# Performance work log

Measured on AMD Instinct MI355X. Metric: run time of the kernel, lower is better.

## Reference

```python
import jax, jax.numpy as jnp
import numpy as np

HID, HEADS, DH, L, OUT = 128, 8, 16, 2, 64
NQ, NA, E, IN = 50000, 50000, 400000, 128
SCALE = float(1.0 / np.sqrt(DH))


def _seg_softmax(alpha, dst, n):
    # softmax over incoming edges of each destination node
    amax = jax.ops.segment_max(alpha, dst, num_segments=n)
    ex = jnp.exp(alpha - amax[dst])
    den = jax.ops.segment_sum(ex, dst, num_segments=n)
    return ex / den[dst]


def _msg(k_src, v_src, q_dst, ei, ar, mr, pr, n_dst):
    # HGTConv message passing for one edge type.
    src, dst = ei[0], ei[1]
    ke = jnp.einsum('ehd,hdf->ehf', k_src[src], ar)  # relation-specific key transform [E,H,DH]
    ve = jnp.einsum('ehd,hdf->ehf', v_src[src], mr)  # relation-specific value transform [E,H,DH]
    alpha = (q_dst[dst] * ke).sum(-1) * pr * SCALE   # [E,H]
    attn = _seg_softmax(alpha, dst, n_dst)
    return jax.ops.segment_sum(attn[..., None] * ve, dst, num_segments=n_dst)  # [n_dst,H,DH]


def setup_inputs():
    key = jax.random.key(0)
    ks = jax.random.split(key, 24)
    f = lambda k, shp: jax.random.normal(k, shp, jnp.float32) * 0.05
    zb = lambda shp: jnp.zeros(shp, jnp.float32)
    return dict(
        x_q=jax.random.normal(ks[0], (NQ, IN), jnp.float32),
        x_a=jax.random.normal(ks[1], (NA, IN), jnp.float32),
        lin0_wq=f(ks[2], (IN, HID)), lin0_bq=zb((HID,)),
        lin0_wa=f(ks[3], (IN, HID)), lin0_ba=zb((HID,)),
        kw_q=f(ks[4], (L, HID, HID)), kb_q=zb((L, HID)),
        qw_q=f(ks[5], (L, HID, HID)), qb_q=zb((L, HID)),
        vw_q=f(ks[6], (L, HID, HID)), vb_q=zb((L, HID)),
        aw_q=f(ks[7], (L, HID, HID)), ab_q=zb((L, HID)),
        kw_a=f(ks[8], (L, HID, HID)), kb_a=zb((L, HID)),
        qw_a=f(ks[9], (L, HID, HID)), qb_a=zb((L, HID)),
        vw_a=f(ks[10], (L, HID, HID)), vb_a=zb((L, HID)),
        aw_a=f(ks[11], (L, HID, HID)), ab_a=zb((L, HID)),
        skip_q=jnp.ones((L,), jnp.float32),
        skip_a=jnp.ones((L,), jnp.float32),
        a_rel=f(ks[12], (L, 2, HEADS, DH, DH)) + jnp.eye(DH, dtype=jnp.float32),
        m_rel=f(ks[13], (L, 2, HEADS, DH, DH)) + jnp.eye(DH, dtype=jnp.float32),
        p_rel=jnp.ones((L, 2, HEADS), jnp.float32),
        lin_w=f(ks[14], (HID, OUT)), lin_b=zb((OUT,)),
        ei_qa=jax.random.randint(ks[15], (2, E), 0, NQ),
        ei_aq=jax.random.randint(ks[16], (2, E), 0, NA),
    )


def reference(x_q, x_a, lin0_wq, lin0_bq, lin0_wa, lin0_ba,
              kw_q, kb_q, qw_q, qb_q, vw_q, vb_q, aw_q, ab_q,
              kw_a, kb_a, qw_a, qb_a, vw_a, vb_a, aw_a, ab_a,
              skip_q, skip_a, a_rel, m_rel, p_rel, lin_w, lin_b,
              ei_qa, ei_aq):
    # per-type input projection + relu
    xq = jax.nn.relu(x_q @ lin0_wq + lin0_bq)
    xa = jax.nn.relu(x_a @ lin0_wa + lin0_ba)
    for l in range(L):
        kq = (xq @ kw_q[l] + kb_q[l]).reshape(NQ, HEADS, DH)
        qq = (xq @ qw_q[l] + qb_q[l]).reshape(NQ, HEADS, DH)
        vq = (xq @ vw_q[l] + vb_q[l]).reshape(NQ, HEADS, DH)
        ka = (xa @ kw_a[l] + kb_a[l]).reshape(NA, HEADS, DH)
        qa = (xa @ qw_a[l] + qb_a[l]).reshape(NA, HEADS, DH)
        va = (xa @ vw_a[l] + vb_a[l]).reshape(NA, HEADS, DH)
        # edge type 0: question -> answer ; edge type 1: answer -> question; group='sum'
        out_a = _msg(kq, vq, qa, ei_qa, a_rel[l, 0], m_rel[l, 0], p_rel[l, 0], NA).reshape(NA, HID)
        out_q = _msg(ka, va, qq, ei_aq, a_rel[l, 1], m_rel[l, 1], p_rel[l, 1], NQ).reshape(NQ, HID)
        oq = jax.nn.gelu(out_q, approximate=False) @ aw_q[l] + ab_q[l]
        oa = jax.nn.gelu(out_a, approximate=False) @ aw_a[l] + ab_a[l]
        gq = jax.nn.sigmoid(skip_q[l])
        ga = jax.nn.sigmoid(skip_a[l])
        xq = gq * oq + (1.0 - gq) * xq
        xa = ga * oa + (1.0 - ga) * xa
    zq = xq @ lin_w + lin_b
    za = xa @ lin_w + lin_b
    # z_dict concatenated: rows [0,NQ) = question, [NQ,NQ+NA) = answer
    return jnp.concatenate([zq, za], axis=0)
```

## Files before the change

### kernel.cpp

```cpp
#include <hip/hip_runtime.h>
#include <hip/hip_bf16.h>
#include <math.h>

typedef __attribute__((ext_vector_type(8))) _Float16 half8;
typedef __attribute__((ext_vector_type(4))) float f32x4;
typedef unsigned short u16;
typedef unsigned int u32;

__device__ __forceinline__ u16 f2h(float f) {
    union { _Float16 h; u16 u; } c; c.h = (_Float16)f; return c.u;
}
__device__ __forceinline__ float h2f(u16 u) {
    union { u16 u; _Float16 h; } c; c.u = u; return (float)c.h;
}
__device__ __forceinline__ float bf2f(u16 u) {
    union { u32 i; float f; } x; x.i = ((u32)u) << 16; return x.f;
}
__device__ __forceinline__ u16 f2bf(float f) {
    union { float f; u32 i; } u; u.f = f;
    u32 r = u.i + 0x7fffu + ((u.i >> 16) & 1u);
    return (u16)(r >> 16);
}
__device__ __forceinline__ float dotpair(u32 a, u32 b) {
    union { u32 i; float f; } alo, ahi, blo, bhi;
    alo.i = a << 16; ahi.i = a & 0xffff0000u;
    blo.i = b << 16; bhi.i = b & 0xffff0000u;
    return alo.f * blo.f + ahi.f * bhi.f;
}
__device__ __forceinline__ int swz_idx(int m, int k) {
    return ((((m >> 4) * 4 + (k >> 5)) * 4 + ((k >> 3) & 3)) * 16 + (m & 15)) * 8 + (k & 7);
}

struct TJob { const float* src; u16* hi; u16* lo; int M; };
struct TJobs { TJob j[10]; };

__global__ void prep_wt_all_k(TJobs jobs) {
    TJob t = jobs.j[blockIdx.y];
    int idx = blockIdx.x * 256 + threadIdx.x;
    if (idx >= t.M * 128) return;
    int m = idx >> 7, k = idx & 127;
    float w = t.src[k * t.M + m];
    u16 h = f2h(w);
    int o = swz_idx(m, k);
    t.hi[o] = h;
    t.lo[o] = f2h(w - h2f(h));
}

__global__ void prep_fused_k(const float* kw_q, const float* kw_a,
                             const float* vw_q, const float* vw_a,
                             const float* a_rel, const float* m_rel,
                             u16* WQh, u16* WQl, u16* WAh, u16* WAl) {
    int j = blockIdx.y;
    int l = j >> 2, dir = (j >> 1) & 1, kv = j & 1;
    const float* w = kv ? (dir ? vw_a : vw_q) : (dir ? kw_a : kw_q);
    w += l * 16384;
    const float* rel = (kv ? m_rel : a_rel) + (l * 2 + dir) * 2048;
    u16* dhi = (dir ? WAh : WQh) + (l * 3 + kv) * 16384;
    u16* dlo = (dir ? WAl : WQl) + (l * 3 + kv) * 16384;
    int idx = blockIdx.x * 256 + threadIdx.x;
    int m = idx >> 7, k = idx & 127;
    int h = m >> 4, f = m & 15;
    float s = 0.f;
#pragma unroll
    for (int d = 0; d < 16; d++)
        s += w[k * 128 + h * 16 + d] * rel[(h * 16 + d) * 16 + f];
    u16 hh = f2h(s);
    int o = swz_idx(m, k);
    dhi[o] = hh;
    dlo[o] = f2h(s - h2f(hh));
}

__global__ void prep_bias_k(const float* kb_q, const float* vb_q, const float* qb_q,
                            const float* kb_a, const float* vb_a, const float* qb_a,
                            const float* a_rel, const float* m_rel,
                            float* BQ, float* BA) {
    int idx = blockIdx.x * 256 + threadIdx.x;
    if (idx >= 1536) return;
    int side = idx / 768, r = idx % 768;
    int l = r / 384, m = r % 384;
    float* dst = side ? BA : BQ;
    if (m >= 256) {
        const float* qb = side ? qb_a : qb_q;
        dst[l * 384 + m] = qb[l * 128 + (m - 256)];
        return;
    }
    int kv = m >> 7, mc = m & 127, h = mc >> 4, f = mc & 15;
    const float* b = side ? (kv ? vb_a : kb_a) : (kv ? vb_q : kb_q);
    b += l * 128;
    const float* rel = (kv ? m_rel : a_rel) + (l * 2 + side) * 2048;
    float s = 0.f;
#pragma unroll
    for (int d = 0; d < 16; d++) s += b[h * 16 + d] * rel[(h * 16 + d) * 16 + f];
    dst[l * 384 + m] = s;
}

__global__ void prep_out_k(const float* aw_q, const float* ab_q, const float* skip_q,
                           const float* aw_a, const float* ab_a, const float* skip_a,
                           const float* lin_w, const float* lin_b,
                           u16* W1h, u16* W1l, u16* W2h, u16* W2l, float* bO) {
    int side = blockIdx.y;
    const float* aw = (side ? aw_a : aw_q) + 16384;
    const float* ab = (side ? ab_a : ab_q) + 128;
    float gk = (side ? skip_a : skip_q)[1];
    float g = 1.f / (1.f + __expf(-gk));
    int idx = blockIdx.x * 256 + threadIdx.x;
    if (idx >= 8192) return;
    int k = idx >> 6, m = idx & 63;
    float s = 0.f;
#pragma unroll 4
    for (int d = 0; d < 128; d++) s += aw[k * 128 + d] * lin_w[d * 64 + m];
    s *= g;
    int o = swz_idx(m, k);
    u16 hh = f2h(s);
    W1h[side * 8192 + o] = hh;
    W1l[side * 8192 + o] = f2h(s - h2f(hh));
    float w2 = (1.f - g) * lin_w[k * 64 + m];
    u16 h2v = f2h(w2);
    W2h[side * 8192 + o] = h2v;
    W2l[side * 8192 + o] = f2h(w2 - h2f(h2v));
    if (k == 0) {
        float b = 0.f;
#pragma unroll 4
        for (int d = 0; d < 128; d++) b += ab[d] * lin_w[d * 64 + m];
        bO[side * 64 + m] = g * b + lin_b[m];
    }
}

__global__ void hist2_k(const int* dA, int Ea, int* degA,
                        const int* dB, int Eb, int* degB) {
    int y = blockIdx.y;
    const int* dst = y ? dB : dA; int E = y ? Eb : Ea; int* deg = y ? degB : degA;
    int i = blockIdx.x * 256 + threadIdx.x;
    if (i < E) atomicAdd(&deg[dst[i]], 1);
}
__global__ void scanA2_k(const int* degA, int* inclA, int* bsumA, int nA,
                         const int* degB, int* inclB, int* bsumB, int nB) {
    int y = blockIdx.y;
    const int* deg = y ? degB : degA; int* incl = y ? inclB : inclA;
    int* bsum = y ? bsumB : bsumA; int n = y ? nB : nA;
    __shared__ int s[256];
    int i = blockIdx.x * 256 + threadIdx.x;
    int v = (i < n) ? deg[i] : 0;
    s[threadIdx.x] = v;
    __syncthreads();
    for (int off = 1; off < 256; off <<= 1) {
        int t = (threadIdx.x >= off) ? s[threadIdx.x - off] : 0;
        __syncthreads();
        s[threadIdx.x] += t;
        __syncthreads();
    }
    if (i < n) incl[i] = s[threadIdx.x];
    if (threadIdx.x == 255) bsum[blockIdx.x] = s[255];
}
__global__ void scanB2_k(int* bsumA, int nbA, int* bsumB, int nbB) {
    int* bsum = blockIdx.x ? bsumB : bsumA;
    int nb = blockIdx.x ? nbB : nbA;
    __shared__ int s[256];
    int v = (threadIdx.x < nb) ? bsum[threadIdx.x] : 0;
    s[threadIdx.x] = v;
    __syncthreads();
    for (int off = 1; off < 256; off <<= 1) {
        int t = (threadIdx.x >= off) ? s[threadIdx.x - off] : 0;
        __syncthreads();
        s[threadIdx.x] += t;
        __syncthreads();
    }
    if (threadIdx.x < nb) bsum[threadIdx.x] = s[threadIdx.x] - v;
}
__global__ void scanC2_k(const int* inclA, const int* degA, const int* bsumA,
                         int* offsA, int* curA, int nA, int Ea,
                         const int* inclB, const int* degB, const int* bsumB,
                         int* offsB, int* curB, int nB, int Eb) {
    int y = blockIdx.y;
    const int* incl = y ? inclB : inclA; const int* deg = y ? degB : degA;
    const int* bsum = y ? bsumB : bsumA;
    int* offs = y ? offsB : offsA; int* cur = y ? curB : curA;
    int n = y ? nB : nA; int E = y ? Eb : Ea;
    int i = blockIdx.x * 256 + threadIdx.x;
    if (i < n) {
        int o = incl[i] - deg[i] + bsum[blockIdx.x];
        offs[i] = o;
        cur[i] = o;
    }
    if (i == 0) offs[n] = E;
}
__global__ void scatter2_k(const int* eiA, int Ea, int* curA, int* srccA,
                           const int* eiB, int Eb, int* curB, int* srccB) {
    int y = blockIdx.y;
    const int* ei = y ? eiB : eiA; int E = y ? Eb : Ea;
    int* cur = y ? curB : curA; int* srcc = y ? srccB : srccA;
    int e = blockIdx.x * 256 + threadIdx.x;
    if (e < E) {
        int p = atomicAdd(&cur[ei[E + e]], 1);
        srcc[p] = ei[e];
    }
}

struct EJob {
    const int* offs; const int* srcc;
    const u16* kt; const u16* vt; const u16* qd;
    const float* pr;
    u16* mhi; int n;
};
struct EJobs { EJob j[2]; };

__global__ __launch_bounds__(256) void edge_fused_k(EJobs jobs) {
    EJob J = jobs.j[blockIdx.y];
    int lane = threadIdx.x & 63;
    int node = blockIdx.x * 4 + (threadIdx.x >> 6);
    if (node >= J.n) return;
    int s0 = J.offs[node], s1 = J.offs[node + 1];
    int h = lane & 7, jj = lane >> 3;
    int hc = lane >> 3;

    float accx = 0.f, accy = 0.f, den = 0.f;

    if (s0 < s1) {
        const u16* qrow = J.qd + (size_t)node * 128 + h * 16;
        uint4 q0 = *(const uint4*)qrow;
        uint4 q1 = *(const uint4*)(qrow + 8);
        float prh = J.pr[h] * 0.25f;

        int jf = s0 + jj;
        int src_next = J.srcc[(jf < s1) ? jf : (s1 - 1)];
        for (int base = s0; base < s1; base += 8) {
            int cnt = s1 - base; if (cnt > 8) cnt = 8;
            int src = src_next;
            if (base + 8 < s1) {
                int jn = base + 8 + jj;
                src_next = J.srcc[(jn < s1) ? jn : (s1 - 1)];
            }
            const u16* krow = J.kt + (size_t)src * 128 + h * 16;
            uint4 k0 = *(const uint4*)krow;
            uint4 k1 = *(const uint4*)(krow + 8);
            float a = dotpair(k0.x, q0.x) + dotpair(k0.y, q0.y)
                    + dotpair(k0.z, q0.z) + dotpair(k0.w, q0.w)
                    + dotpair(k1.x, q1.x) + dotpair(k1.y, q1.y)
                    + dotpair(k1.z, q1.z) + dotpair(k1.w, q1.w);
            float p = (jj < cnt) ? __expf(a * prh) : 0.f;
            den += p;

            u32 vv[8];
#pragma unroll
            for (int t = 0; t < 8; t++) {
                int s2 = __shfl(src, t * 8);
                vv[t] = (t < cnt) ? *(const u32*)(J.vt + (size_t)s2 * 128 + lane * 2) : 0u;
            }
#pragma unroll
            for (int t = 0; t < 8; t++) {
                float w = __shfl(p, t * 8 + hc);
                accx += w * bf2f((u16)(vv[t] & 0xffffu));
                accy += w * bf2f((u16)(vv[t] >> 16));
            }
        }
        den += __shfl_xor(den, 8);
        den += __shfl_xor(den, 16);
        den += __shfl_xor(den, 32);
    }

    float dc = __shfl(den, hc);
    float inv = (dc > 0.f) ? (1.f / dc) : 0.f;
    float vx = accx * inv, vy = accy * inv;
    vx = 0.5f * vx * (1.f + erff(vx * 0.70710678118654752f));
    vy = 0.5f * vy * (1.f + erff(vy * 0.70710678118654752f));
    size_t ob = (size_t)node * 128 + lane * 2;
    *(u32*)(J.mhi + ob) = (u32)f2h(vx) | ((u32)f2h(vy) << 16);
}


struct GJob3 { const u16* xhi; const u16* wh; const float* bias;
               u16* y0; u16* y1; u16* y2; int N; };
struct GJobs3 { GJob3 j[2]; };

__global__ __launch_bounds__(256, 3) void gemm_proj3_k(GJobs3 jobs) {
    GJob3 J = jobs.j[blockIdx.y];
    int tid = threadIdx.x;
    int wave = tid >> 6, lane = tid & 63;
    int lr = lane & 15, kg = lane >> 4;
    u16* const ys[3] = {J.y0, J.y1, J.y2};

    half8 wh[3][2][4];
#pragma unroll
    for (int c = 0; c < 3; c++)
#pragma unroll
        for (int ct = 0; ct < 2; ct++)
#pragma unroll
            for (int ks = 0; ks < 4; ks++) {
                int o = c * 16384 + ((wave * 2 + ct) * 4 + ks) * 512 + kg * 128 + lr * 8;
                wh[c][ct][ks] = *(const half8*)(J.wh + o);
            }

    int N = J.N;
    int ntiles = (N + 15) >> 4;
    for (int t = blockIdx.x; t < ntiles; t += gridDim.x) {
        int arow = t * 16 + lr;
        if (arow >= N) arow = N - 1;
        const u16* ph = J.xhi + (size_t)arow * 128 + kg * 8;
        half8 ah[4];
#pragma unroll
        for (int ks = 0; ks < 4; ks++) ah[ks] = *(const half8*)(ph + ks * 32);

        int crow0 = t * 16 + kg * 4;
#pragma unroll
        for (int c = 0; c < 3; c++) {
            f32x4 acc[2] = {f32x4{0.f, 0.f, 0.f, 0.f}, f32x4{0.f, 0.f, 0.f, 0.f}};
#pragma unroll
            for (int ks = 0; ks < 4; ks++)
#pragma unroll
                for (int ct = 0; ct < 2; ct++)
                    acc[ct] = __builtin_amdgcn_mfma_f32_16x16x32_f16(ah[ks], wh[c][ct][ks], acc[ct], 0, 0, 0);
#pragma unroll
            for (int ct = 0; ct < 2; ct++) {
                int col = (wave * 2 + ct) * 16 + lr;
                float bcol = J.bias[c * 128 + col];
#pragma unroll
                for (int r = 0; r < 4; r++) {
                    int gr = crow0 + r;
                    if (gr < N) ys[c][(size_t)gr * 128 + col] = f2bf(acc[ct][r] + bcol);
                }
            }
        }
    }
}

struct SJob { const u16* mhi; const u16* wh; const u16* wl;
              const float* bias; u16* xhi; const float* gate; int N; };
struct SJobs { SJob j[2]; };

__global__ __launch_bounds__(256, 4) void gemm_skip_k(SJobs jobs) {
    SJob J = jobs.j[blockIdx.y];
    int tid = threadIdx.x;
    int wave = tid >> 6, lane = tid & 63;
    int lr = lane & 15, kg = lane >> 4;

    half8 wh[2][4], wl[2][4];
#pragma unroll
    for (int ct = 0; ct < 2; ct++)
#pragma unroll
        for (int ks = 0; ks < 4; ks++) {
            int o = ((wave * 2 + ct) * 4 + ks) * 512 + kg * 128 + lr * 8;
            wh[ct][ks] = *(const half8*)(J.wh + o);
            wl[ct][ks] = *(const half8*)(J.wl + o);
        }
    float gk = J.gate[0];
    float g = 1.f / (1.f + __expf(-gk));
    float gi = 1.f - g;

    int ntiles = (J.N + 15) >> 4;
    for (int t = blockIdx.x; t < ntiles; t += gridDim.x) {
        int arow = t * 16 + lr;
        if (arow >= J.N) arow = J.N - 1;
        const u16* ph = J.mhi + (size_t)arow * 128 + kg * 8;
        half8 ah[4];
#pragma unroll
        for (int ks = 0; ks < 4; ks++) ah[ks] = *(const half8*)(ph + ks * 32);
        f32x4 acc[2] = {f32x4{0.f, 0.f, 0.f, 0.f}, f32x4{0.f, 0.f, 0.f, 0.f}};
#pragma unroll
        for (int ks = 0; ks < 4; ks++)
#pragma unroll
            for (int ct = 0; ct < 2; ct++) {
                acc[ct] = __builtin_amdgcn_mfma_f32_16x16x32_f16(ah[ks], wh[ct][ks], acc[ct], 0, 0, 0);
                acc[ct] = __builtin_amdgcn_mfma_f32_16x16x32_f16(ah[ks], wl[ct][ks], acc[ct], 0, 0, 0);
            }
        int crow0 = t * 16 + kg * 4;
#pragma unroll
        for (int ct = 0; ct < 2; ct++) {
            int col = (wave * 2 + ct) * 16 + lr;
            float bcol = J.bias[col];
#pragma unroll
            for (int r = 0; r < 4; r++) {
                int gr = crow0 + r;
                if (gr < J.N) {
                    size_t si = (size_t)gr * 128 + col;
                    float v = acc[ct][r] + bcol;
                    v = g * v + gi * h2f(J.xhi[si]);
                    J.xhi[si] = f2h(v);
                }
            }
        }
    }
}

struct FJob { const float* x; const u16* wh; const u16* wl; const float* bias;
              u16* yhi; int N; };
struct FJobs { FJob j[2]; };

__global__ __launch_bounds__(256, 3) void gemm_in_k(FJobs jobs) {
    FJob J = jobs.j[blockIdx.y];
    int tid = threadIdx.x;
    int wave = tid >> 6, lane = tid & 63;
    int lr = lane & 15, kg = lane >> 4;

    half8 wh[2][4], wl[2][4];
#pragma unroll
    for (int ct = 0; ct < 2; ct++)
#pragma unroll
        for (int ks = 0; ks < 4; ks++) {
            int o = ((wave * 2 + ct) * 4 + ks) * 512 + kg * 128 + lr * 8;
            wh[ct][ks] = *(const half8*)(J.wh + o);
            wl[ct][ks] = *(const half8*)(J.wl + o);
        }

    int ntiles = (J.N + 15) >> 4;
    for (int t = blockIdx.x; t < ntiles; t += gridDim.x) {
        int arow = t * 16 + lr;
        if (arow >= J.N) arow = J.N - 1;
        const float* p = J.x + (size_t)arow * 128 + kg * 8;
        half8 ahi[4], alo[4];
#pragma unroll
        for (int ks = 0; ks < 4; ks++) {
            float4 v0 = *(const float4*)(p + ks * 32);
            float4 v1 = *(const float4*)(p + ks * 32 + 4);
            float a8[8] = {v0.x, v0.y, v0.z, v0.w, v1.x, v1.y, v1.z, v1.w};
#pragma unroll
            for (int j = 0; j < 8; j++) {
                _Float16 h = (_Float16)a8[j];
                ahi[ks][j] = h;
                alo[ks][j] = (_Float16)(a8[j] - (float)h);
            }
        }
        f32x4 acc[2] = {f32x4{0.f, 0.f, 0.f, 0.f}, f32x4{0.f, 0.f, 0.f, 0.f}};
#pragma unroll
        for (int ks = 0; ks < 4; ks++)
#pragma unroll
            for (int ct = 0; ct < 2; ct++) {
                acc[ct] = __builtin_amdgcn_mfma_f32_16x16x32_f16(ahi[ks], wh[ct][ks], acc[ct], 0, 0, 0);
                acc[ct] = __builtin_amdgcn_mfma_f32_16x16x32_f16(alo[ks], wh[ct][ks], acc[ct], 0, 0, 0);
                acc[ct] = __builtin_amdgcn_mfma_f32_16x16x32_f16(ahi[ks], wl[ct][ks], acc[ct], 0, 0, 0);
            }
        int crow0 = t * 16 + kg * 4;
#pragma unroll
        for (int ct = 0; ct < 2; ct++) {
            int col = (wave * 2 + ct) * 16 + lr;
            float bcol = J.bias[col];
#pragma unroll
            for (int r = 0; r < 4; r++) {
                int gr = crow0 + r;
                if (gr < J.N) {
                    float v = fmaxf(acc[ct][r] + bcol, 0.f);
                    J.yhi[(size_t)gr * 128 + col] = f2h(v);
                }
            }
        }
    }
}

struct OJob { const u16* mhi; const u16* xhi;
              const u16* w1h; const u16* w1l; const u16* w2h; const u16* w2l;
              const float* bO; float* out; int N; };
struct OJobs { OJob j[2]; };

__global__ __launch_bounds__(256, 4) void gemm_out_k(OJobs jobs) {
    OJob J = jobs.j[blockIdx.y];
    int tid = threadIdx.x;
    int wave = tid >> 6, lane = tid & 63;
    int lr = lane & 15, kg = lane >> 4;

    half8 w1h[4], w1l[4], w2h[4], w2l[4];
#pragma unroll
    for (int ks = 0; ks < 4; ks++) {
        int o = (wave * 4 + ks) * 512 + kg * 128 + lr * 8;
        w1h[ks] = *(const half8*)(J.w1h + o);
        w1l[ks] = *(const half8*)(J.w1l + o);
        w2h[ks] = *(const half8*)(J.w2h + o);
        w2l[ks] = *(const half8*)(J.w2l + o);
    }

    int N = J.N;
    int ntiles = (N + 15) >> 4;
    for (int t = blockIdx.x; t < ntiles; t += gridDim.x) {
        int arow = t * 16 + lr;
        if (arow >= N) arow = N - 1;
        const u16* pm = J.mhi + (size_t)arow * 128 + kg * 8;
        const u16* px = J.xhi + (size_t)arow * 128 + kg * 8;
        half8 am[4], ax[4];
#pragma unroll
        for (int ks = 0; ks < 4; ks++) {
            am[ks] = *(const half8*)(pm + ks * 32);
            ax[ks] = *(const half8*)(px + ks * 32);
        }
        f32x4 acc = f32x4{0.f, 0.f, 0.f, 0.f};
#pragma unroll
        for (int ks = 0; ks < 4; ks++) {
            acc = __builtin_amdgcn_mfma_f32_16x16x32_f16(am[ks], w1h[ks], acc, 0, 0, 0);
            acc = __builtin_amdgcn_mfma_f32_16x16x32_f16(am[ks], w1l[ks], acc, 0, 0, 0);
            acc = __builtin_amdgcn_mfma_f32_16x16x32_f16(ax[ks], w2h[ks], acc, 0, 0, 0);
            acc = __builtin_amdgcn_mfma_f32_16x16x32_f16(ax[ks], w2l[ks], acc, 0, 0, 0);
        }
        int crow0 = t * 16 + kg * 4;
        int col = wave * 16 + lr;
        float bcol = J.bO[col];
#pragma unroll
        for (int r = 0; r < 4; r++) {
            int gr = crow0 + r;
            if (gr < N) J.out[(size_t)gr * 64 + col] = acc[r] + bcol;
        }
    }
}

extern "C" void kernel_launch(void* const* d_in, const int* in_sizes, int n_in,
                              void* d_out, int out_size, void* d_ws, size_t ws_size,
                              hipStream_t stream) {
    const int NQ = in_sizes[0] / 128;
    const int NA = in_sizes[1] / 128;
    const int Eqa = in_sizes[29] / 2;
    const int Eaq = in_sizes[30] / 2;
    const int NM = (NQ > NA) ? NQ : NA;
    const int EM = (Eqa > Eaq) ? Eqa : Eaq;

    const float* x_q     = (const float*)d_in[0];
    const float* x_a     = (const float*)d_in[1];
    const float* lin0_wq = (const float*)d_in[2];
    const float* lin0_bq = (const float*)d_in[3];
    const float* lin0_wa = (const float*)d_in[4];
    const float* lin0_ba = (const float*)d_in[5];
    const float* kw_q = (const float*)d_in[6];
    const float* kb_q = (const float*)d_in[7];
    const float* qw_q = (const float*)d_in[8];
    const float* qb_q = (const float*)d_in[9];
    const float* vw_q = (const float*)d_in[10];
    const float* vb_q = (const float*)d_in[11];
    const float* aw_q = (const float*)d_in[12];
    const float* ab_q = (const float*)d_in[13];
    const float* kw_a = (const float*)d_in[14];
    const float* kb_a = (const float*)d_in[15];
    const float* qw_a = (const float*)d_in[16];
    const float* qb_a = (const float*)d_in[17];
    const float* vw_a = (const float*)d_in[18];
    const float* vb_a = (const float*)d_in[19];
    const float* aw_a = (const float*)d_in[20];
    const float* ab_a = (const float*)d_in[21];
    const float* skip_q = (const float*)d_in[22];
    const float* skip_a = (const float*)d_in[23];
    const float* a_rel = (const float*)d_in[24];
    const float* m_rel = (const float*)d_in[25];
    const float* p_rel = (const float*)d_in[26];
    const float* lin_w = (const float*)d_in[27];
    const float* lin_b = (const float*)d_in[28];
    const int* ei_qa = (const int*)d_in[29];
    const int* ei_aq = (const int*)d_in[30];

    size_t off = 0;
    auto alloc = [&](size_t bytes) -> void* {
        void* p = (char*)d_ws + off;
        off += (bytes + 255) & ~(size_t)255;
        return p;
    };
    u16* xhi = (u16*)alloc((size_t)(NQ + NA) * 128 * 2);
    u16* xq_hi = xhi;
    u16* xa_hi = xhi + (size_t)NQ * 128;
    u16* mq_hi = (u16*)alloc((size_t)NQ * 128 * 2);
    u16* ma_hi = (u16*)alloc((size_t)NA * 128 * 2);
    u16* kt0 = (u16*)alloc((size_t)NM * 128 * 2);
    u16* vt0 = (u16*)alloc((size_t)NM * 128 * 2);
    u16* qdq = (u16*)alloc((size_t)NM * 128 * 2);
    u16* kt1 = (u16*)alloc((size_t)NM * 128 * 2);
    u16* vt1 = (u16*)alloc((size_t)NM * 128 * 2);
    u16* qda = (u16*)alloc((size_t)NM * 128 * 2);
    int* offs_a = (int*)alloc((size_t)(NA + 1) * 4);
    int* offs_q = (int*)alloc((size_t)(NQ + 1) * 4);
    int* srcc_a = (int*)alloc((size_t)Eqa * 4);
    int* srcc_q = (int*)alloc((size_t)Eaq * 4);
    int* deg    = (int*)alloc((size_t)2 * NM * 4);
    int* cursor = (int*)alloc((size_t)2 * NM * 4);
    int* incl   = (int*)alloc((size_t)2 * NM * 4);
    int* bsum   = (int*)alloc(2048);
    u16* W_LIN0Q_h = (u16*)alloc(16384 * 2); u16* W_LIN0Q_l = (u16*)alloc(16384 * 2);
    u16* W_LIN0A_h = (u16*)alloc(16384 * 2); u16* W_LIN0A_l = (u16*)alloc(16384 * 2);
    u16* WQ_h = (u16*)alloc(2 * 3 * 16384 * 2); u16* WQ_l = (u16*)alloc(2 * 3 * 16384 * 2);
    u16* WA_h = (u16*)alloc(2 * 3 * 16384 * 2); u16* WA_l = (u16*)alloc(2 * 3 * 16384 * 2);
    u16* W_AQ_h = (u16*)alloc(2 * 16384 * 2); u16* W_AQ_l = (u16*)alloc(2 * 16384 * 2);
    u16* W_AA_h = (u16*)alloc(2 * 16384 * 2); u16* W_AA_l = (u16*)alloc(2 * 16384 * 2);
    u16* W1h = (u16*)alloc(2 * 8192 * 2); u16* W1l = (u16*)alloc(2 * 8192 * 2);
    u16* W2h = (u16*)alloc(2 * 8192 * 2); u16* W2l = (u16*)alloc(2 * 8192 * 2);
    float* bO = (float*)alloc(2 * 64 * 4);
    float* BQ = (float*)alloc(2 * 384 * 4);
    float* BA = (float*)alloc(2 * 384 * 4);
    (void)ws_size; (void)n_in; (void)out_size; (void)EM;

    dim3 B(256);

    TJobs tj;
    tj.j[0]  = {lin0_wq, W_LIN0Q_h, W_LIN0Q_l, 128};
    tj.j[1]  = {lin0_wa, W_LIN0A_h, W_LIN0A_l, 128};
    tj.j[2]  = {qw_q,          WQ_h + (0 * 3 + 2) * 16384, WQ_l + (0 * 3 + 2) * 16384, 128};
    tj.j[3]  = {qw_q + 16384,  WQ_h + (1 * 3 + 2) * 16384, WQ_l + (1 * 3 + 2) * 16384, 128};
    tj.j[4]  = {qw_a,          WA_h + (0 * 3 + 2) * 16384, WA_l + (0 * 3 + 2) * 16384, 128};
    tj.j[5]  = {qw_a + 16384,  WA_h + (1 * 3 + 2) * 16384, WA_l + (1 * 3 + 2) * 16384, 128};
    tj.j[6]  = {aw_q,          W_AQ_h,            W_AQ_l,            128};
    tj.j[7]  = {aw_q + 16384,  W_AQ_h + 16384,    W_AQ_l + 16384,    128};
    tj.j[8]  = {aw_a,          W_AA_h,            W_AA_l,            128};
    tj.j[9]  = {aw_a + 16384,  W_AA_h + 16384,    W_AA_l + 16384,    128};
    prep_wt_all_k<<<dim3(64, 10), B, 0, stream>>>(tj);
    prep_fused_k<<<dim3(64, 8), B, 0, stream>>>(kw_q, kw_a, vw_q, vw_a, a_rel, m_rel,
                                                WQ_h, WQ_l, WA_h, WA_l);
    prep_bias_k<<<dim3(6), B, 0, stream>>>(kb_q, vb_q, qb_q, kb_a, vb_a, qb_a,
                                           a_rel, m_rel, BQ, BA);
    prep_out_k<<<dim3(32, 2), B, 0, stream>>>(aw_q, ab_q, skip_q, aw_a, ab_a, skip_a,
                                              lin_w, lin_b, W1h, W1l, W2h, W2l, bO);

    int* degA = deg;        int* degB = deg + NM;
    int* curA = cursor;     int* curB = cursor + NM;
    int* incA = incl;       int* incB = incl + NM;
    int* bsA  = bsum;       int* bsB  = bsum + 256;
    int gEm = (EM + 255) / 256, gNm = (NM + 255) / 256;
    int gNa = (NA + 255) / 256, gNq = (NQ + 255) / 256;
    hipMemsetAsync(deg, 0, (size_t)2 * NM * 4, stream);
    hist2_k<<<dim3(gEm, 2), B, 0, stream>>>(ei_qa + Eqa, Eqa, degA, ei_aq + Eaq, Eaq, degB);
    scanA2_k<<<dim3(gNm, 2), B, 0, stream>>>(degA, incA, bsA, NA, degB, incB, bsB, NQ);
    scanB2_k<<<dim3(2), B, 0, stream>>>(bsA, gNa, bsB, gNq);
    scanC2_k<<<dim3(gNm, 2), B, 0, stream>>>(incA, degA, bsA, offs_a, curA, NA, Eqa,
                                             incB, degB, bsB, offs_q, curB, NQ, Eaq);
    scatter2_k<<<dim3(gEm, 2), B, 0, stream>>>(ei_qa, Eqa, curA, srcc_a,
                                               ei_aq, Eaq, curB, srcc_q);

    {
        FJobs fj;
        fj.j[0] = {x_q, W_LIN0Q_h, W_LIN0Q_l, lin0_bq, xq_hi, NQ};
        fj.j[1] = {x_a, W_LIN0A_h, W_LIN0A_l, lin0_ba, xa_hi, NA};
        gemm_in_k<<<dim3(512, 2), B, 0, stream>>>(fj);
    }

    for (int l = 0; l < 2; l++) {
        GJobs3 gj;
        gj.j[0] = {xq_hi, WQ_h + l * 3 * 16384, BQ + l * 384, kt0, vt0, qdq, NQ};
        gj.j[1] = {xa_hi, WA_h + l * 3 * 16384, BA + l * 384, kt1, vt1, qda, NA};
        gemm_proj3_k<<<dim3(512, 2), B, 0, stream>>>(gj);

        EJobs ej;
        ej.j[0] = {offs_a, srcc_a, kt0, vt0, qda, p_rel + (l * 2 + 0) * 8, ma_hi, NA};
        ej.j[1] = {offs_q, srcc_q, kt1, vt1, qdq, p_rel + (l * 2 + 1) * 8, mq_hi, NQ};
        edge_fused_k<<<dim3((NM + 3) / 4, 2), B, 0, stream>>>(ej);

        if (l == 0) {
            SJobs sj;
            sj.j[0] = {mq_hi, W_AQ_h, W_AQ_l, ab_q, xq_hi, skip_q, NQ};
            sj.j[1] = {ma_hi, W_AA_h, W_AA_l, ab_a, xa_hi, skip_a, NA};
            gemm_skip_k<<<dim3(512, 2), B, 0, stream>>>(sj);
        } else {
            OJobs oj;
            oj.j[0] = {mq_hi, xq_hi, W1h, W1l, W2h, W2l, bO,
                       (float*)d_out, NQ};
            oj.j[1] = {ma_hi, xa_hi, W1h + 8192, W1l + 8192, W2h + 8192, W2l + 8192, bO + 64,
                       (float*)d_out + (size_t)NQ * 64, NA};
            gemm_out_k<<<dim3(512, 2), B, 0, stream>>>(oj);
        }
    }
}
```

Baseline: 414.0 us.

## Merge weight-prep kernels into one launch and double GEMM grid sizes

Combines the two weight preprocessing kernels (transpose/split and relation-fused weights) into a single launch dispatched on blockIdx.y, removing one kernel launch. It also doubles the grid x-dimension of the four GEMM kernels from 512 to 1024 blocks, presumably to spread the 50k-row work over more workgroups. This gives better load balance at the cost of more per-block setup such as weight staging, assuming the kernels use grid-stride loops over row tiles.

```diff
diff --git a/kernel.cpp b/kernel.cpp
--- a/kernel.cpp
+++ b/kernel.cpp
@@ -32,32 +32,34 @@
 }
 
 struct TJob { const float* src; u16* hi; u16* lo; int M; };
-struct TJobs { TJob j[10]; };
-
-__global__ void prep_wt_all_k(TJobs jobs) {
-    TJob t = jobs.j[blockIdx.y];
+struct PrepArgs {
+    TJob j[10];
+    const float* kw_q; const float* kw_a; const float* vw_q; const float* vw_a;
+    const float* a_rel; const float* m_rel;
+    u16* WQh; u16* WQl; u16* WAh; u16* WAl;
+};
+
+__global__ void prep_all_k(PrepArgs A) {
+    int y = blockIdx.y;
     int idx = blockIdx.x * 256 + threadIdx.x;
-    if (idx >= t.M * 128) return;
-    int m = idx >> 7, k = idx & 127;
-    float w = t.src[k * t.M + m];
-    u16 h = f2h(w);
-    int o = swz_idx(m, k);
-    t.hi[o] = h;
-    t.lo[o] = f2h(w - h2f(h));
-}
-
-__global__ void prep_fused_k(const float* kw_q, const float* kw_a,
-                             const float* vw_q, const float* vw_a,
-                             const float* a_rel, const float* m_rel,
-                             u16* WQh, u16* WQl, u16* WAh, u16* WAl) {
-    int j = blockIdx.y;
+    if (y < 10) {
+        TJob t = A.j[y];
+        if (idx >= t.M * 128) return;
+        int m = idx >> 7, k = idx & 127;
+        float w = t.src[k * t.M + m];
+        u16 h = f2h(w);
+        int o = swz_idx(m, k);
+        t.hi[o] = h;
+        t.lo[o] = f2h(w - h2f(h));
+        return;
+    }
+    int j = y - 10;
     int l = j >> 2, dir = (j >> 1) & 1, kv = j & 1;
-    const float* w = kv ? (dir ? vw_a : vw_q) : (dir ? kw_a : kw_q);
+    const float* w = kv ? (dir ? A.vw_a : A.vw_q) : (dir ? A.kw_a : A.kw_q);
     w += l * 16384;
-    const float* rel = (kv ? m_rel : a_rel) + (l * 2 + dir) * 2048;
-    u16* dhi = (dir ? WAh : WQh) + (l * 3 + kv) * 16384;
-    u16* dlo = (dir ? WAl : WQl) + (l * 3 + kv) * 16384;
-    int idx = blockIdx.x * 256 + threadIdx.x;
+    const float* rel = (kv ? A.m_rel : A.a_rel) + (l * 2 + dir) * 2048;
+    u16* dhi = (dir ? A.WAh : A.WQh) + (l * 3 + kv) * 16384;
+    u16* dlo = (dir ? A.WAl : A.WQl) + (l * 3 + kv) * 16384;
     int m = idx >> 7, k = idx & 127;
     int h = m >> 4, f = m & 15;
     float s = 0.f;
@@ -580,20 +582,21 @@
 
     dim3 B(256);
 
-    TJobs tj;
-    tj.j[0]  = {lin0_wq, W_LIN0Q_h, W_LIN0Q_l, 128};
-    tj.j[1]  = {lin0_wa, W_LIN0A_h, W_LIN0A_l, 128};
-    tj.j[2]  = {qw_q,          WQ_h + (0 * 3 + 2) * 16384, WQ_l + (0 * 3 + 2) * 16384, 128};
-    tj.j[3]  = {qw_q + 16384,  WQ_h + (1 * 3 + 2) * 16384, WQ_l + (1 * 3 + 2) * 16384, 128};
-    tj.j[4]  = {qw_a,          WA_h + (0 * 3 + 2) * 16384, WA_l + (0 * 3 + 2) * 16384, 128};
-    tj.j[5]  = {qw_a + 16384,  WA_h + (1 * 3 + 2) * 16384, WA_l + (1 * 3 + 2) * 16384, 128};
-    tj.j[6]  = {aw_q,          W_AQ_h,            W_AQ_l,            128};
-    tj.j[7]  = {aw_q + 16384,  W_AQ_h + 16384,    W_AQ_l + 16384,    128};
-    tj.j[8]  = {aw_a,          W_AA_h,            W_AA_l,            128};
-    tj.j[9]  = {aw_a + 16384,  W_AA_h + 16384,    W_AA_l + 16384,    128};
-    prep_wt_all_k<<<dim3(64, 10), B, 0, stream>>>(tj);
-    prep_fused_k<<<dim3(64, 8), B, 0, stream>>>(kw_q, kw_a, vw_q, vw_a, a_rel, m_rel,
-                                                WQ_h, WQ_l, WA_h, WA_l);
+    PrepArgs pa;
+    pa.j[0]  = {lin0_wq, W_LIN0Q_h, W_LIN0Q_l, 128};
+    pa.j[1]  = {lin0_wa, W_LIN0A_h, W_LIN0A_l, 128};
+    pa.j[2]  = {qw_q,          WQ_h + (0 * 3 + 2) * 16384, WQ_l + (0 * 3 + 2) * 16384, 128};
+    pa.j[3]  = {qw_q + 16384,  WQ_h + (1 * 3 + 2) * 16384, WQ_l + (1 * 3 + 2) * 16384, 128};
+    pa.j[4]  = {qw_a,          WA_h + (0 * 3 + 2) * 16384, WA_l + (0 * 3 + 2) * 16384, 128};
+    pa.j[5]  = {qw_a + 16384,  WA_h + (1 * 3 + 2) * 16384, WA_l + (1 * 3 + 2) * 16384, 128};
+    pa.j[6]  = {aw_q,          W_AQ_h,            W_AQ_l,            128};
+    pa.j[7]  = {aw_q + 16384,  W_AQ_h + 16384,    W_AQ_l + 16384,    128};
+    pa.j[8]  = {aw_a,          W_AA_h,            W_AA_l,            128};
+    pa.j[9]  = {aw_a + 16384,  W_AA_h + 16384,    W_AA_l + 16384,    128};
+    pa.kw_q = kw_q; pa.kw_a = kw_a; pa.vw_q = vw_q; pa.vw_a = vw_a;
+    pa.a_rel = a_rel; pa.m_rel = m_rel;
+    pa.WQh = WQ_h; pa.WQl = WQ_l; pa.WAh = WA_h; pa.WAl = WA_l;
+    prep_all_k<<<dim3(64, 18), B, 0, stream>>>(pa);
     prep_bias_k<<<dim3(6), B, 0, stream>>>(kb_q, vb_q, qb_q, kb_a, vb_a, qb_a,
                                            a_rel, m_rel, BQ, BA);
     prep_out_k<<<dim3(32, 2), B, 0, stream>>>(aw_q, ab_q, skip_q, aw_a, ab_a, skip_a,
@@ -618,14 +621,14 @@
         FJobs fj;
         fj.j[0] = {x_q, W_LIN0Q_h, W_LIN0Q_l, lin0_bq, xq_hi, NQ};
         fj.j[1] = {x_a, W_LIN0A_h, W_LIN0A_l, lin0_ba, xa_hi, NA};
-        gemm_in_k<<<dim3(512, 2), B, 0, stream>>>(fj);
+        gemm_in_k<<<dim3(1024, 2), B, 0, stream>>>(fj);
     }
 
     for (int l = 0; l < 2; l++) {
         GJobs3 gj;
         gj.j[0] = {xq_hi, WQ_h + l * 3 * 16384, BQ + l * 384, kt0, vt0, qdq, NQ};
         gj.j[1] = {xa_hi, WA_h + l * 3 * 16384, BA + l * 384, kt1, vt1, qda, NA};
-        gemm_proj3_k<<<dim3(512, 2), B, 0, stream>>>(gj);
+        gemm_proj3_k<<<dim3(1024, 2), B, 0, stream>>>(gj);
 
         EJobs ej;
         ej.j[0] = {offs_a, srcc_a, kt0, vt0, qda, p_rel + (l * 2 + 0) * 8, ma_hi, NA};
@@ -636,14 +639,14 @@
             SJobs sj;
             sj.j[0] = {mq_hi, W_AQ_h, W_AQ_l, ab_q, xq_hi, skip_q, NQ};
             sj.j[1] = {ma_hi, W_AA_h, W_AA_l, ab_a, xa_hi, skip_a, NA};
-            gemm_skip_k<<<dim3(512, 2), B, 0, stream>>>(sj);
+            gemm_skip_k<<<dim3(1024, 2), B, 0, stream>>>(sj);
         } else {
             OJobs oj;
             oj.j[0] = {mq_hi, xq_hi, W1h, W1l, W2h, W2l, bO,
                        (float*)d_out, NQ};
             oj.j[1] = {ma_hi, xa_hi, W1h + 8192, W1l + 8192, W2h + 8192, W2l + 8192, bO + 64,
                        (float*)d_out + (size_t)NQ * 64, NA};
-            gemm_out_k<<<dim3(512, 2), B, 0, stream>>>(oj);
-        }
-    }
-}
+            gemm_out_k<<<dim3(1024, 2), B, 0, stream>>>(oj);
+        }
+    }
+}
```

Result: no change. 408.7 us (-1.3%).
